# Performance work log

Measured on AMD Instinct MI355X. Metric: run time of the kernel, lower is better.

The kernel has to match this reference:

```python
import jax, jax.numpy as jnp
import numpy as np
import math

V, D, H, L, T, B = 32000, 768, 12, 4, 1024, 2
HD = D // H  # head size 64
EMB_SCALE = math.sqrt(D)  # DynamicTanh path
EPS = 1e-5


def setup_inputs() -> dict:
    key = jax.random.key(0)
    ks = jax.random.split(key, 10)
    def rn(k, shape, std=0.02):
        return jax.random.normal(k, shape, jnp.float32) * std
    return {
        "idx": jax.random.randint(ks[0], (B, T), 0, V, dtype=jnp.int32).astype(jnp.int64) if False else jax.random.randint(ks[0], (B, T), 0, V),
        "wte": rn(ks[1], (V, D)),            # tied with lm_head
        "wpe": rn(ks[2], (T, D)),            # block_size == T
        "ln1_alpha": jnp.full((L, 1), 0.5, jnp.float32),
        "ln1_w": jnp.ones((L, D), jnp.float32),
        "ln1_b": jnp.zeros((L, D), jnp.float32),
        "wq": rn(ks[3], (L, D, D)),          # stored [in,out] (torch W.T)
        "wk": rn(ks[4], (L, D, D)),
        "wv": rn(ks[5], (L, D, D)),
        "wo": rn(ks[6], (L, D, D)),
        "bo": jnp.zeros((L, D), jnp.float32),
        "ln2_alpha": jnp.full((L, 1), 0.5, jnp.float32),
        "ln2_w": jnp.ones((L, D), jnp.float32),
        "ln2_b": jnp.zeros((L, D), jnp.float32),
        "w_fc": rn(ks[7], (L, D, 4 * D)),
        "b_fc": jnp.zeros((L, 4 * D), jnp.float32),
        "w_proj": rn(ks[8], (L, 4 * D, D), std=0.02 / math.sqrt(2 * L)),
        "b_proj": jnp.zeros((L, D), jnp.float32),
        "lnf_alpha": jnp.full((1,), 0.5, jnp.float32),
        "lnf_w": jnp.ones((D,), jnp.float32),
        "lnf_b": jnp.zeros((D,), jnp.float32),
    }


def _dyt(x, alpha, w, b):
    # DynamicTanh: layernorm-style normalize, then w * tanh(alpha * xn) + b
    mu = x.mean(-1, keepdims=True)
    var = ((x - mu) ** 2).mean(-1, keepdims=True)
    xn = (x - mu) * jax.lax.rsqrt(var + EPS)
    return w * jnp.tanh(alpha * xn) + b


def reference(idx, wte, wpe, ln1_alpha, ln1_w, ln1_b, wq, wk, wv, wo, bo,
              ln2_alpha, ln2_w, ln2_b, w_fc, b_fc, w_proj, b_proj,
              lnf_alpha, lnf_w, lnf_b):
    Bb, Tt = idx.shape
    x = (wte[idx] + wpe[:Tt][None]) * EMB_SCALE          # [B,T,D]; dropout = eval identity
    mask = jnp.tril(jnp.ones((Tt, Tt), bool))
    scale = 1.0 / math.sqrt(HD)
    for l in range(L):
        h = _dyt(x, ln1_alpha[l], ln1_w[l], ln1_b[l])
        q = (h @ wq[l]).reshape(Bb, Tt, H, HD)
        k = (h @ wk[l]).reshape(Bb, Tt, H, HD)
        v = (h @ wv[l]).reshape(Bb, Tt, H, HD)
        att = jnp.einsum('bqhd,bkhd->bhqk', q, k) * scale
        att = jnp.where(mask, att, -jnp.inf)
        att = jax.nn.softmax(att, axis=-1)
        o = jnp.einsum('bhqk,bkhd->bqhd', att, v).reshape(Bb, Tt, D)
        x = x + o @ wo[l] + bo[l]
        h = _dyt(x, ln2_alpha[l], ln2_w[l], ln2_b[l])
        h = jax.nn.gelu(h @ w_fc[l] + b_fc[l], approximate=False)  # torch nn.GELU = exact erf
        x = x + h @ w_proj[l] + b_proj[l]
    x = _dyt(x, lnf_alpha, lnf_w, lnf_b)
    return x @ wte.T                                     # tied lm_head, [B,T,V]
```

## Files before the change

### kernel.cpp

```cpp
#include <hip/hip_runtime.h>
#include <hip/hip_bf16.h>
#include <math.h>

constexpr int B_ = 2, T_ = 1024, D_ = 768, H_ = 12, L_ = 4, V_ = 32000;
constexpr int M_ = B_ * T_;
constexpr int FF_ = 4 * D_;
constexpr int QKVN_ = 3 * D_;
#define EMB_SCALE 27.712812921102035f
#define EPS_ 1e-5f

typedef __attribute__((ext_vector_type(8))) short short8_t;
typedef __attribute__((ext_vector_type(4))) float float4_t;

__device__ __forceinline__ float bf2f(__hip_bfloat16 v) { return __bfloat162float(v); }
__device__ __forceinline__ __hip_bfloat16 f2bf(float v) { return __float2bfloat16(v); }

__device__ __forceinline__ void gl_lds16(const __hip_bfloat16* g, __hip_bfloat16* l) {
    __builtin_amdgcn_global_load_lds(
        (const __attribute__((address_space(1))) void*)g,
        (__attribute__((address_space(3))) void*)l, 16, 0, 0);
}

__global__ __launch_bounds__(256) void convert_kernel(
    const float* __restrict__ src, __hip_bfloat16* __restrict__ dst, size_t n)
{
    size_t i = ((size_t)blockIdx.x * 256 + threadIdx.x) * 4;
    if (i + 3 < n) {
        float4 f = *(const float4*)(src + i);
        dst[i + 0] = f2bf(f.x);
        dst[i + 1] = f2bf(f.y);
        dst[i + 2] = f2bf(f.z);
        dst[i + 3] = f2bf(f.w);
    }
}

__global__ __launch_bounds__(256) void tconv_kernel(
    const float* __restrict__ src, __hip_bfloat16* __restrict__ dst,
    int K, int N, size_t sstride, size_t dstride)
{
    __shared__ float tile[32][33];
    const float* S = src + (size_t)blockIdx.z * sstride;
    __hip_bfloat16* Dd = dst + (size_t)blockIdx.z * dstride;
    int n0 = blockIdx.x * 32, k0 = blockIdx.y * 32;
    int tx = threadIdx.x & 31, ty = threadIdx.x >> 5;
#pragma unroll
    for (int i = 0; i < 32; i += 8)
        tile[ty + i][tx] = S[(size_t)(k0 + ty + i) * N + n0 + tx];
    __syncthreads();
#pragma unroll
    for (int i = 0; i < 32; i += 8)
        Dd[(size_t)(n0 + ty + i) * K + k0 + tx] = f2bf(tile[tx][ty + i]);
}

__global__ __launch_bounds__(256) void embed_kernel(
    const int* __restrict__ idx, const float* __restrict__ wte,
    const float* __restrict__ wpe, float* __restrict__ x)
{
    int row = blockIdx.x, tid = threadIdx.x;
    int t = row & (T_ - 1);
    int tok = idx[row];
#pragma unroll
    for (int i = 0; i < 3; ++i) {
        int c = i * 256 + tid;
        x[(size_t)row * D_ + c] =
            (wte[(size_t)tok * D_ + c] + wpe[(size_t)t * D_ + c]) * EMB_SCALE;
    }
}

__global__ __launch_bounds__(256) void dyt_kernel(
    const float* __restrict__ x, __hip_bfloat16* __restrict__ h,
    const float* __restrict__ w, const float* __restrict__ bb,
    const float* __restrict__ alpha_p)
{
    const int row = blockIdx.x, tid = threadIdx.x;
    const float* xr = x + (size_t)row * D_;
    float v[3];
    float s = 0.f, ss = 0.f;
#pragma unroll
    for (int i = 0; i < 3; ++i) {
        v[i] = xr[i * 256 + tid];
        s += v[i];
        ss += v[i] * v[i];
    }
#pragma unroll
    for (int off = 32; off >= 1; off >>= 1) {
        s  += __shfl_xor(s,  off, 64);
        ss += __shfl_xor(ss, off, 64);
    }
    __shared__ float sh[8];
    int wave = tid >> 6;
    if ((tid & 63) == 0) { sh[wave] = s; sh[wave + 4] = ss; }
    __syncthreads();
    s  = sh[0] + sh[1] + sh[2] + sh[3];
    ss = sh[4] + sh[5] + sh[6] + sh[7];
    float mu = s * (1.f / D_);
    float var = ss * (1.f / D_) - mu * mu;
    float rstd = rsqrtf(var + EPS_);
    float alpha = *alpha_p;
#pragma unroll
    for (int i = 0; i < 3; ++i) {
        int c = i * 256 + tid;
        float xn = (v[i] - mu) * rstd;
        h[(size_t)row * D_ + c] = f2bf(w[c] * tanhf(alpha * xn) + bb[c]);
    }
}

constexpr int LSTR = 72;

__global__ __launch_bounds__(256) void fattn_kernel(
    const __hip_bfloat16* __restrict__ qkv, __hip_bfloat16* __restrict__ o)
{
    const int qt = gridDim.x - 1 - blockIdx.x;
    const int hh = blockIdx.y, b = blockIdx.z;
    const int q0 = qt * 64;
    const int tid = threadIdx.x;
    const int wave = tid >> 6, lane = tid & 63;
    const int quad = lane >> 4, l16 = lane & 15;
    const size_t rs = QKVN_;

    __shared__ __hip_bfloat16 Ks[64 * LSTR];
    __shared__ __hip_bfloat16 Vts[64 * LSTR];
    __shared__ __hip_bfloat16 Ps[4][16 * LSTR];

    const __hip_bfloat16* qrow = qkv + (size_t)(b * T_ + q0 + wave * 16 + l16) * rs + hh * 64;
    short8_t qf0 = *(const short8_t*)(qrow + quad * 8);
    short8_t qf1 = *(const short8_t*)(qrow + 32 + quad * 8);

    float4_t Oacc[4];
#pragma unroll
    for (int j = 0; j < 4; ++j) Oacc[j] = (float4_t){0.f, 0.f, 0.f, 0.f};
    float mrow[4], lrow[4];
#pragma unroll
    for (int r = 0; r < 4; ++r) { mrow[r] = -1e30f; lrow[r] = 0.f; }

    const __hip_bfloat16* kbase = qkv + (size_t)b * T_ * rs + D_ + hh * 64;
    const __hip_bfloat16* vbase = qkv + (size_t)b * T_ * rs + 2 * D_ + hh * 64;

    const int sr = tid >> 2;
    const int sc = (tid & 3) * 8;
    const int vr = lane;
    const int vc0 = wave * 16;

    for (int kt = 0; kt <= qt; ++kt) {
        const int kt0 = kt * 64;
        uint4 kv0 = *(const uint4*)(kbase + (size_t)(kt0 + sr) * rs + sc);
        uint4 kv1 = *(const uint4*)(kbase + (size_t)(kt0 + sr) * rs + sc + 32);
        uint4 vv0 = *(const uint4*)(vbase + (size_t)(kt0 + vr) * rs + vc0);
        uint4 vv1 = *(const uint4*)(vbase + (size_t)(kt0 + vr) * rs + vc0 + 8);
        __syncthreads();
        *(uint4*)(Ks + sr * LSTR + sc)      = kv0;
        *(uint4*)(Ks + sr * LSTR + sc + 32) = kv1;
        {
            const __hip_bfloat16* vp = (const __hip_bfloat16*)&vv0;
#pragma unroll
            for (int i = 0; i < 8; ++i) Vts[(vc0 + i) * LSTR + vr] = vp[i];
            vp = (const __hip_bfloat16*)&vv1;
#pragma unroll
            for (int i = 0; i < 8; ++i) Vts[(vc0 + 8 + i) * LSTR + vr] = vp[i];
        }
        __syncthreads();

        float4_t S[4];
#pragma unroll
        for (int jt = 0; jt < 4; ++jt) {
            short8_t kf0 = *(const short8_t*)(Ks + (jt * 16 + l16) * LSTR + quad * 8);
            short8_t kf1 = *(const short8_t*)(Ks + (jt * 16 + l16) * LSTR + 32 + quad * 8);
            float4_t s = (float4_t){0.f, 0.f, 0.f, 0.f};
            s = __builtin_amdgcn_mfma_f32_16x16x32_bf16(qf0, kf0, s, 0, 0, 0);
            s = __builtin_amdgcn_mfma_f32_16x16x32_bf16(qf1, kf1, s, 0, 0, 0);
            S[jt] = s;
        }

        if (kt == qt) {
#pragma unroll
            for (int jt = 0; jt < 4; ++jt)
#pragma unroll
                for (int r = 0; r < 4; ++r) {
                    int qg = wave * 16 + quad * 4 + r;
                    int kg = jt * 16 + l16;
                    S[jt][r] = (kg > qg) ? -1e30f : S[jt][r] * 0.125f;
                }
        } else {
#pragma unroll
            for (int jt = 0; jt < 4; ++jt)
#pragma unroll
                for (int r = 0; r < 4; ++r) S[jt][r] *= 0.125f;
        }

        float mnew[4], alphav[4];
#pragma unroll
        for (int r = 0; r < 4; ++r) {
            float mx = fmaxf(fmaxf(S[0][r], S[1][r]), fmaxf(S[2][r], S[3][r]));
            mx = fmaxf(mx, __shfl_xor(mx, 1, 64));
            mx = fmaxf(mx, __shfl_xor(mx, 2, 64));
            mx = fmaxf(mx, __shfl_xor(mx, 4, 64));
            mx = fmaxf(mx, __shfl_xor(mx, 8, 64));
            mnew[r] = fmaxf(mrow[r], mx);
            alphav[r] = __expf(mrow[r] - mnew[r]);
            mrow[r] = mnew[r];
        }
        float psum[4] = {0.f, 0.f, 0.f, 0.f};
#pragma unroll
        for (int jt = 0; jt < 4; ++jt)
#pragma unroll
            for (int r = 0; r < 4; ++r) {
                float p = __expf(S[jt][r] - mnew[r]);
                S[jt][r] = p;
                psum[r] += p;
            }
#pragma unroll
        for (int r = 0; r < 4; ++r) {
            float ps = psum[r];
            ps += __shfl_xor(ps, 1, 64);
            ps += __shfl_xor(ps, 2, 64);
            ps += __shfl_xor(ps, 4, 64);
            ps += __shfl_xor(ps, 8, 64);
            lrow[r] = lrow[r] * alphav[r] + ps;
        }

        __hip_bfloat16* ps_base = Ps[wave];
#pragma unroll
        for (int jt = 0; jt < 4; ++jt)
#pragma unroll
            for (int r = 0; r < 4; ++r)
                ps_base[(quad * 4 + r) * LSTR + jt * 16 + l16] = f2bf(S[jt][r]);

#pragma unroll
        for (int j = 0; j < 4; ++j)
#pragma unroll
            for (int r = 0; r < 4; ++r) Oacc[j][r] *= alphav[r];

        short8_t pf0 = *(const short8_t*)(ps_base + l16 * LSTR + quad * 8);
        short8_t pf1 = *(const short8_t*)(ps_base + l16 * LSTR + 32 + quad * 8);
#pragma unroll
        for (int j = 0; j < 4; ++j) {
            short8_t vf0 = *(const short8_t*)(Vts + (j * 16 + l16) * LSTR + quad * 8);
            short8_t vf1 = *(const short8_t*)(Vts + (j * 16 + l16) * LSTR + 32 + quad * 8);
            Oacc[j] = __builtin_amdgcn_mfma_f32_16x16x32_bf16(pf0, vf0, Oacc[j], 0, 0, 0);
            Oacc[j] = __builtin_amdgcn_mfma_f32_16x16x32_bf16(pf1, vf1, Oacc[j], 0, 0, 0);
        }
    }

    float inv_l[4];
#pragma unroll
    for (int r = 0; r < 4; ++r) inv_l[r] = 1.f / lrow[r];
    __hip_bfloat16* orow = o + (size_t)(b * T_ + q0 + wave * 16) * D_ + hh * 64;
#pragma unroll
    for (int j = 0; j < 4; ++j)
#pragma unroll
        for (int r = 0; r < 4; ++r)
            orow[(size_t)(quad * 4 + r) * D_ + j * 16 + l16] = f2bf(Oacc[j][r] * inv_l[r]);
}

__device__ __forceinline__ float gelu_exact(float t) {
    return 0.5f * t * (1.0f + erff(t * 0.70710678118654752f));
}

template <int EPI>
__global__ __launch_bounds__(256, 2) void gemm_bt(
    const __hip_bfloat16* __restrict__ A, const __hip_bfloat16* __restrict__ Bt,
    float* __restrict__ outF, __hip_bfloat16* __restrict__ outB,
    const float* __restrict__ bias, const float* __restrict__ res,
    int M, int N, int K)
{
    __shared__ __hip_bfloat16 As[128 * 32];
    __shared__ __hip_bfloat16 Bs[128 * 32];
    const int tid = threadIdx.x;
    const int wave = tid >> 6, lane = tid & 63;
    const int quad = lane >> 4, l16 = lane & 15;
    const int m0 = blockIdx.y * 128, n0 = blockIdx.x * 128;
    const int wm = (wave >> 1) * 64, wn = (wave & 1) * 64;

    float4_t acc[4][4];
#pragma unroll
    for (int i = 0; i < 4; ++i)
#pragma unroll
        for (int j = 0; j < 4; ++j) acc[i][j] = (float4_t){0.f, 0.f, 0.f, 0.f};

    const int lr = lane >> 2, lc = (lane & 3) * 8;
    const __hip_bfloat16* ga0 = A  + (size_t)(m0 + wave * 16 + lr) * K + lc;
    const __hip_bfloat16* ga1 = A  + (size_t)(m0 + 64 + wave * 16 + lr) * K + lc;
    const __hip_bfloat16* gb0 = Bt + (size_t)(n0 + wave * 16 + lr) * K + lc;
    const __hip_bfloat16* gb1 = Bt + (size_t)(n0 + 64 + wave * 16 + lr) * K + lc;
    __hip_bfloat16* la0 = As + (wave * 16) * 32;
    __hip_bfloat16* la1 = As + (64 + wave * 16) * 32;
    __hip_bfloat16* lb0 = Bs + (wave * 16) * 32;
    __hip_bfloat16* lb1 = Bs + (64 + wave * 16) * 32;

    for (int k0 = 0; k0 < K; k0 += 32) {
        __syncthreads();
        gl_lds16(ga0 + k0, la0);
        gl_lds16(ga1 + k0, la1);
        gl_lds16(gb0 + k0, lb0);
        gl_lds16(gb1 + k0, lb1);
        __syncthreads();
        short8_t af[4], bfv[4];
#pragma unroll
        for (int i = 0; i < 4; ++i) {
            af[i]  = *(const short8_t*)(As + (wm + i * 16 + l16) * 32 + quad * 8);
            bfv[i] = *(const short8_t*)(Bs + (wn + i * 16 + l16) * 32 + quad * 8);
        }
#pragma unroll
        for (int i = 0; i < 4; ++i)
#pragma unroll
            for (int j = 0; j < 4; ++j)
                acc[i][j] = __builtin_amdgcn_mfma_f32_16x16x32_bf16(
                    af[i], bfv[j], acc[i][j], 0, 0, 0);
    }

#pragma unroll
    for (int i = 0; i < 4; ++i) {
#pragma unroll
        for (int j = 0; j < 4; ++j) {
            int colg = n0 + wn + j * 16 + l16;
#pragma unroll
            for (int rg = 0; rg < 4; ++rg) {
                int rowg = m0 + wm + i * 16 + quad * 4 + rg;
                size_t offo = (size_t)rowg * N + colg;
                float v = acc[i][j][rg];
                if (EPI == 0) {
                    outB[offo] = f2bf(v);
                } else if (EPI == 1) {
                    outF[offo] = res[offo] + v + bias[colg];
                } else if (EPI == 2) {
                    outB[offo] = f2bf(gelu_exact(v + bias[colg]));
                } else {
                    outF[offo] = v;
                }
            }
        }
    }
}

extern "C" void kernel_launch(void* const* d_in, const int* in_sizes, int n_in,
                              void* d_out, int out_size, void* d_ws, size_t ws_size,
                              hipStream_t stream)
{
    const int*   idx   = (const int*)d_in[0];
    const float* wte   = (const float*)d_in[1];
    const float* wpe   = (const float*)d_in[2];
    const float* ln1_a = (const float*)d_in[3];
    const float* ln1_w = (const float*)d_in[4];
    const float* ln1_b = (const float*)d_in[5];
    const float* wq    = (const float*)d_in[6];
    const float* wk    = (const float*)d_in[7];
    const float* wv    = (const float*)d_in[8];
    const float* wo    = (const float*)d_in[9];
    const float* bo    = (const float*)d_in[10];
    const float* ln2_a = (const float*)d_in[11];
    const float* ln2_w = (const float*)d_in[12];
    const float* ln2_b = (const float*)d_in[13];
    const float* w_fc  = (const float*)d_in[14];
    const float* b_fc  = (const float*)d_in[15];
    const float* w_pr  = (const float*)d_in[16];
    const float* b_pr  = (const float*)d_in[17];
    const float* lnf_a = (const float*)d_in[18];
    const float* lnf_w = (const float*)d_in[19];
    const float* lnf_b = (const float*)d_in[20];
    float* out = (float*)d_out;

    char* ws = (char*)d_ws;
    size_t off = 0;
    auto alloc = [&](size_t bytes) -> char* {
        char* p = ws + off;
        off += (bytes + 255) & ~(size_t)255;
        return p;
    };
    __hip_bfloat16* wqkv_t = (__hip_bfloat16*)alloc((size_t)L_ * QKVN_ * D_ * 2);
    __hip_bfloat16* wo_t   = (__hip_bfloat16*)alloc((size_t)L_ * D_ * D_ * 2);
    __hip_bfloat16* wfc_t  = (__hip_bfloat16*)alloc((size_t)L_ * FF_ * D_ * 2);
    __hip_bfloat16* wpr_t  = (__hip_bfloat16*)alloc((size_t)L_ * D_ * FF_ * 2);
    __hip_bfloat16* wte_b  = (__hip_bfloat16*)alloc((size_t)V_ * D_ * 2);
    float*          x      = (float*)alloc((size_t)M_ * D_ * 4);
    __hip_bfloat16* h      = (__hip_bfloat16*)alloc((size_t)M_ * D_ * 2);
    __hip_bfloat16* qkv    = (__hip_bfloat16*)alloc((size_t)M_ * QKVN_ * 2);
    __hip_bfloat16* attno  = (__hip_bfloat16*)alloc((size_t)M_ * D_ * 2);
    __hip_bfloat16* mid    = (__hip_bfloat16*)alloc((size_t)M_ * FF_ * 2);
    (void)ws_size; (void)in_sizes; (void)n_in; (void)out_size;

    {
        size_t n = (size_t)V_ * D_;
        convert_kernel<<<dim3((unsigned)(n / 1024)), 256, 0, stream>>>(wte, wte_b, n);
    }
    size_t wstride = (size_t)D_ * D_;
    tconv_kernel<<<dim3(24, 24, L_), 256, 0, stream>>>(wq, wqkv_t + 0,            D_, D_, wstride, (size_t)QKVN_ * D_);
    tconv_kernel<<<dim3(24, 24, L_), 256, 0, stream>>>(wk, wqkv_t + (size_t)D_ * D_,   D_, D_, wstride, (size_t)QKVN_ * D_);
    tconv_kernel<<<dim3(24, 24, L_), 256, 0, stream>>>(wv, wqkv_t + (size_t)2 * D_ * D_, D_, D_, wstride, (size_t)QKVN_ * D_);
    tconv_kernel<<<dim3(24, 24, L_), 256, 0, stream>>>(wo, wo_t,                  D_, D_, wstride, wstride);
    tconv_kernel<<<dim3(96, 24, L_), 256, 0, stream>>>(w_fc, wfc_t, D_, FF_, (size_t)D_ * FF_, (size_t)FF_ * D_);
    tconv_kernel<<<dim3(24, 96, L_), 256, 0, stream>>>(w_pr, wpr_t, FF_, D_, (size_t)FF_ * D_, (size_t)D_ * FF_);

    embed_kernel<<<dim3(M_), 256, 0, stream>>>(idx, wte, wpe, x);

    for (int l = 0; l < L_; ++l) {
        dyt_kernel<<<dim3(M_), 256, 0, stream>>>(x, h, ln1_w + l * D_, ln1_b + l * D_, ln1_a + l);
        gemm_bt<0><<<dim3(QKVN_ / 128, M_ / 128), 256, 0, stream>>>(
            h, wqkv_t + (size_t)l * QKVN_ * D_, nullptr, qkv, nullptr, nullptr, M_, QKVN_, D_);
        fattn_kernel<<<dim3(T_ / 64, H_, B_), 256, 0, stream>>>(qkv, attno);
        gemm_bt<1><<<dim3(D_ / 128, M_ / 128), 256, 0, stream>>>(
            attno, wo_t + (size_t)l * D_ * D_, x, nullptr, bo + l * D_, x, M_, D_, D_);
        dyt_kernel<<<dim3(M_), 256, 0, stream>>>(x, h, ln2_w + l * D_, ln2_b + l * D_, ln2_a + l);
        gemm_bt<2><<<dim3(FF_ / 128, M_ / 128), 256, 0, stream>>>(
            h, wfc_t + (size_t)l * FF_ * D_, nullptr, mid, b_fc + l * FF_, nullptr, M_, FF_, D_);
        gemm_bt<1><<<dim3(D_ / 128, M_ / 128), 256, 0, stream>>>(
            mid, wpr_t + (size_t)l * D_ * FF_, x, nullptr, b_pr + l * D_, x, M_, D_, FF_);
    }

    dyt_kernel<<<dim3(M_), 256, 0, stream>>>(x, h, lnf_w, lnf_b, lnf_a);
    gemm_bt<3><<<dim3(V_ / 128, M_ / 128), 256, 0, stream>>>(
        h, wte_b, out, nullptr, nullptr, nullptr, M_, V_, D_);
}
```

Measured before the change: 1.306 ms.

## Add dedicated 256x256-tile LM-head GEMM with LDS swizzle and async pipelining

Replaces the generic 128x128 gemm_bt for the vocabulary projection with a specialized kernel. It uses 256x256 tiles over 512 threads, direct global-to-LDS loads with an XOR swizzle, double buffering split into half-tiles, and a grouped block ordering for L2 reuse. The goal is more data reuse and better overlap of loads with MFMA work on the largest GEMM, which dominates runtime. In exchange it adds hand-written waitcnt and barrier logic that is fragile, hardcoded for these dimensions, and carries higher register pressure.

```diff
diff --git a/kernel.cpp b/kernel.cpp
--- a/kernel.cpp
+++ b/kernel.cpp
@@ -330,6 +330,116 @@
             }
         }
     }
+}
+
+__global__ __launch_bounds__(512, 2) void gemm_lmhead(
+    const __hip_bfloat16* __restrict__ A, const __hip_bfloat16* __restrict__ Bt,
+    float* __restrict__ out)
+{
+    constexpr int K = D_;
+    constexpr int N = V_;
+    constexpr int NT = K / 32;
+    __shared__ __hip_bfloat16 lds[32768];
+
+    const int tid  = threadIdx.x;
+    const int wave = tid >> 6, lane = tid & 63;
+    const int quad = lane >> 4, l16 = lane & 15;
+
+    const int flat = blockIdx.x;
+    const int g = (flat & 7) * 125 + (flat >> 3);
+    const int m0 = (g & 7) * 256, n0 = (g >> 3) * 256;
+
+    const int wm = (wave >> 2) * 128;
+    const int wn = (wave & 3) * 64;
+
+    const int slr  = tid >> 2;
+    const int sq   = (tid & 3) ^ ((slr >> 1) & 3);
+    const int rbase = ((slr & 64) << 1) | (slr & 63);
+    const __hip_bfloat16* gA = A  + (size_t)(m0 + rbase) * K + sq * 8;
+    const __hip_bfloat16* gB = Bt + (size_t)(n0 + rbase) * K + sq * 8;
+    const int wb = wave * 1024;
+    char* ldsc = (char*)lds;
+
+#define STG(gp, Xoff, hh, tt) \
+    gl_lds16((gp) + (size_t)(hh) * 64 * K + (tt) * 32, \
+             (__hip_bfloat16*)(ldsc + (((tt) & 1) * 32768 + (Xoff) + (hh) * 8192 + wb)))
+
+    const int xe   = (quad ^ ((l16 >> 1) & 3)) * 16;
+    const int aoff = wm * 32 + l16 * 64 + xe;
+    const int boff = 16384 + ((wn >> 6) & 1) * 8192 + (wn & 128) * 32 + l16 * 64 + xe;
+
+    float4_t acc[8][4];
+#pragma unroll
+    for (int i = 0; i < 8; ++i)
+#pragma unroll
+        for (int j = 0; j < 4; ++j) acc[i][j] = (float4_t){0.f, 0.f, 0.f, 0.f};
+
+    STG(gA, 0,     0, 0); STG(gB, 16384, 0, 0);
+    STG(gA, 0,     1, 0); STG(gB, 16384, 1, 0);
+    STG(gA, 0,     0, 1); STG(gB, 16384, 0, 1);
+    asm volatile("s_waitcnt vmcnt(2)" ::: "memory");
+    __builtin_amdgcn_sched_barrier(0);
+    __builtin_amdgcn_s_barrier();
+
+    auto do_tile = [&](int tt, bool last2) {
+        const char* base = ldsc + (tt & 1) * 32768;
+        short8_t af[4], bf[4];
+#pragma unroll
+        for (int ii = 0; ii < 4; ++ii)
+            af[ii] = *(const short8_t*)(base + ii * 1024 + aoff);
+#pragma unroll
+        for (int j = 0; j < 4; ++j)
+            bf[j] = *(const short8_t*)(base + j * 1024 + boff);
+        if (tt + 1 < NT) { STG(gA, 0, 1, tt + 1); STG(gB, 16384, 1, tt + 1); }
+        __builtin_amdgcn_s_barrier();
+        asm volatile("s_waitcnt lgkmcnt(0)" ::: "memory");
+        __builtin_amdgcn_sched_barrier(0);
+        __builtin_amdgcn_s_setprio(1);
+#pragma unroll
+        for (int ii = 0; ii < 4; ++ii)
+#pragma unroll
+            for (int j = 0; j < 4; ++j)
+                acc[ii][j] = __builtin_amdgcn_mfma_f32_16x16x32_bf16(
+                    af[ii], bf[j], acc[ii][j], 0, 0, 0);
+        __builtin_amdgcn_s_setprio(0);
+        __builtin_amdgcn_s_barrier();
+#pragma unroll
+        for (int ii = 0; ii < 4; ++ii)
+            af[ii] = *(const short8_t*)(base + 8192 + ii * 1024 + aoff);
+        if (tt + 2 < NT) { STG(gA, 0, 0, tt + 2); STG(gB, 16384, 0, tt + 2); }
+        __builtin_amdgcn_s_barrier();
+        asm volatile("s_waitcnt lgkmcnt(0)" ::: "memory");
+        __builtin_amdgcn_sched_barrier(0);
+        __builtin_amdgcn_s_setprio(1);
+#pragma unroll
+        for (int ii = 0; ii < 4; ++ii)
+#pragma unroll
+            for (int j = 0; j < 4; ++j)
+                acc[4 + ii][j] = __builtin_amdgcn_mfma_f32_16x16x32_bf16(
+                    af[ii], bf[j], acc[4 + ii][j], 0, 0, 0);
+        __builtin_amdgcn_s_setprio(0);
+        if (last2) {
+            asm volatile("s_waitcnt vmcnt(0)" ::: "memory");
+        } else {
+            asm volatile("s_waitcnt vmcnt(2)" ::: "memory");
+        }
+        __builtin_amdgcn_sched_barrier(0);
+        __builtin_amdgcn_s_barrier();
+    };
+
+    for (int t = 0; t + 2 < NT; t += 2) { do_tile(t, false); do_tile(t + 1, false); }
+    do_tile(NT - 2, true);
+    do_tile(NT - 1, false);
+#undef STG
+
+    float* orow = out + (size_t)(m0 + wm + quad * 4) * N + (n0 + wn + l16);
+#pragma unroll
+    for (int i = 0; i < 8; ++i)
+#pragma unroll
+        for (int j = 0; j < 4; ++j)
+#pragma unroll
+            for (int rg = 0; rg < 4; ++rg)
+                orow[(size_t)(i * 16 + rg) * N + j * 16] = acc[i][j][rg];
 }
 
 extern "C" void kernel_launch(void* const* d_in, const int* in_sizes, int n_in,
@@ -407,6 +517,5 @@
     }
 
     dyt_kernel<<<dim3(M_), 256, 0, stream>>>(x, h, lnf_w, lnf_b, lnf_a);
-    gemm_bt<3><<<dim3(V_ / 128, M_ / 128), 256, 0, stream>>>(
-        h, wte_b, out, nullptr, nullptr, nullptr, M_, V_, D_);
-}
+    gemm_lmhead<<<dim3((M_ / 256) * (V_ / 256)), 512, 0, stream>>>(h, wte_b, out);
+}
```

Result: faster. 1.275 ms (-2.4%).
